# Optimization experiments

Hardware: AMD Instinct MI355X
Metric: run time of the kernel (lower is better)

The kernel has to match this reference:

```python
import jax, jax.numpy as jnp
import numpy as np

K = 10
NEG_SLOPE = 0.2


def _knn(x, k):
    # x: (B, C, N) -> idx (B, N, k) of k nearest neighbors (smallest sq-dist)
    inner = -2.0 * jnp.einsum('bcn,bcm->bnm', x, x)
    xx = jnp.sum(x * x, axis=1)  # (B, N)
    pd = -xx[:, :, None] - inner - xx[:, None, :]  # negative squared distance
    return jax.lax.top_k(pd, k)[1]


def _gather(xt, idx):
    # xt: (B, N, C), idx: (B, N, k) -> (B, N, k, C)
    return jax.vmap(lambda f, i: f[i])(xt, idx)


def graph_feature(x, k):
    # x: (B, C, N) -> (B, 2C, N, k)
    idx = _knn(x, k)
    xt = jnp.transpose(x, (0, 2, 1))  # (B, N, C)
    feat = _gather(xt, idx)           # (B, N, k, C)
    xc = xt[:, :, None, :]
    out = jnp.concatenate([feat - xc, jnp.broadcast_to(xc, feat.shape)], axis=3)
    return jnp.transpose(out, (0, 3, 1, 2))


def graph_feature1(x, k):
    # knn on first 2 dims (2D coords); x: (B, C, N) -> (B, 2C, N, k)
    idx = _knn(x[:, 0:2, :], k)
    xt = jnp.transpose(x, (0, 2, 1))
    feat = _gather(xt, idx)
    xc = jnp.broadcast_to(xt[:, :, None, :], feat.shape)
    out = jnp.concatenate([feat[..., :2] - xc[..., :2], feat[..., 2:], xc], axis=3)
    return jnp.transpose(out, (0, 3, 1, 2))


def _lrelu(v):
    return jnp.where(v >= 0, v, NEG_SLOPE * v)


def _cbr2(f, W, s, t):
    # 1x1 conv2d + folded-BN + leaky relu; f: (B, C, N, k)
    y = jnp.einsum('oc,bcnk->bonk', W, f)
    return _lrelu(y * s[None, :, None, None] + t[None, :, None, None])


def _cbr1(f, W, s, t):
    # 1x1 conv1d + folded-BN + leaky relu; f: (B, C, N)
    y = jnp.einsum('oc,bcn->bon', W, f)
    return _lrelu(y * s[None, :, None] + t[None, :, None])


def setup_inputs() -> dict:
    key = jax.random.key(0)
    ks = jax.random.split(key, 32)
    B, C, N = 8, 7, 4096
    d = {'x': jax.random.normal(ks[0], (B, C, N), jnp.float32)}
    wshapes = [('W1', (64, 14)), ('W2', (64, 64)), ('W3', (64, 128)), ('W4', (64, 64)),
               ('W5', (64, 128)), ('W6', (256, 192)), ('W7', (512, 448)), ('W8', (128, 1024))]
    for i, (n, s) in enumerate(wshapes):
        d[n] = jax.random.normal(ks[1 + i], s, jnp.float32) * (1.0 / np.sqrt(s[1]))
    bdims = [64, 64, 64, 64, 64, 256, 512, 128]
    for i, c in enumerate(bdims):
        d[f's{i + 1}'] = jax.random.uniform(ks[9 + i], (c,), jnp.float32, 0.5, 1.5)
        d[f't{i + 1}'] = jax.random.normal(ks[17 + i], (c,), jnp.float32) * 0.1
    return d


def reference(x, W1, W2, W3, W4, W5, W6, W7, W8,
              s1, s2, s3, s4, s5, s6, s7, s8,
              t1, t2, t3, t4, t5, t6, t7, t8):
    B, _, N = x.shape
    h = graph_feature1(x, K)              # (B, 14, N, K)
    h = _cbr2(h, W1, s1, t1)
    h = _cbr2(h, W2, s2, t2)
    x1 = h.mean(axis=-1)                  # (B, 64, N)
    h = graph_feature(x1, K)              # (B, 128, N, K)
    h = _cbr2(h, W3, s3, t3)
    h = _cbr2(h, W4, s4, t4)
    x2 = h.mean(axis=-1)
    h = graph_feature(x2, K)
    h = _cbr2(h, W5, s5, t5)
    x3 = h.mean(axis=-1)
    h = jnp.concatenate([x1, x2, x3], axis=1)   # (B, 192, N)
    h = _cbr1(h, W6, s6, t6)                    # (B, 256, N)
    g = h.mean(axis=-1, keepdims=True)          # (B, 256, 1)
    g = jnp.broadcast_to(g, (B, 256, N))
    h = jnp.concatenate([g, x1, x2, x3], axis=1)  # (B, 448, N)
    h = _cbr1(h, W7, s7, t7)                      # (B, 512, N)
    x4 = h.max(axis=-1)
    x5 = h.mean(axis=-1)
    h = jnp.concatenate([x4, x5], axis=1)         # (B, 1024)
    h = h @ W8.T                                  # (B, 128)
    return _lrelu(h * s8[None, :] + t8[None, :])
```

## Files before the change

### kernel.cpp

```cpp
#include <hip/hip_runtime.h>

#define BB 8
#define NN 4096
#define KK 10
#define CAP 24
#define TT 6
typedef unsigned long long u64;
typedef __attribute__((ext_vector_type(8))) short bf16x8;
typedef __attribute__((ext_vector_type(4))) float f32x4;

__device__ __forceinline__ float lrelu(float v){ return v >= 0.f ? v : 0.2f*v; }
__device__ __forceinline__ float bc(float v, int l){
  return __int_as_float(__builtin_amdgcn_readlane(__float_as_int(v), l));
}
__device__ __forceinline__ unsigned fenc(float f){
  unsigned u = __float_as_uint(f);
  return u ^ (((unsigned)((int)u >> 31)) | 0x80000000u);
}
__device__ __forceinline__ float fdec(unsigned e){
  return (e & 0x80000000u) ? __uint_as_float(e & 0x7fffffffu) : __uint_as_float(~e);
}
__device__ __forceinline__ u64 shflx_u64(u64 x, int d){
  unsigned lo = __shfl_xor((unsigned)x, d, 64);
  unsigned hi = __shfl_xor((unsigned)(x >> 32), d, 64);
  return ((u64)hi << 32) | lo;
}

__global__ __launch_bounds__(256) void prep_k(
    const float* __restrict__ W1, const float* __restrict__ W2, const float* __restrict__ W3,
    const float* __restrict__ W4, const float* __restrict__ W5, const float* __restrict__ W8,
    float* __restrict__ W1T, float* __restrict__ W2T, float* __restrict__ W5T, float* __restrict__ W8T,
    unsigned short* __restrict__ W3dh, unsigned short* __restrict__ W3dl,
    unsigned short* __restrict__ W3qh, unsigned short* __restrict__ W3ql,
    unsigned short* __restrict__ W4h,  unsigned short* __restrict__ W4l)
{
  const int t = blockIdx.x*256 + threadIdx.x;
  const int stride = gridDim.x*256;
  for (int i=t; i<64*14; i+=stride){ int o=i/14, c=i%14; W1T[c*64+o]=W1[i]; }
  for (int i=t; i<64*64; i+=stride){ int o=i>>6, c=i&63; W2T[c*64+o]=W2[i]; }
  for (int i=t; i<64*128; i+=stride){ int o=i>>7, c=i&127; W5T[c*64+o]=W5[i]; }
  for (int i=t; i<128*1024; i+=stride){ int o=i>>10, c=i&1023; W8T[c*128+o]=W8[i]; }
  for (int i=t; i<64*64; i+=stride){
    int o=i>>6, c=i&63;
    float f = W3[o*128 + c];
    unsigned u = __float_as_uint(f);
    W3dh[i] = (unsigned short)(u >> 16);
    float lo = f - __uint_as_float(u & 0xffff0000u);
    W3dl[i] = (unsigned short)(__float_as_uint(lo) >> 16);
  }
  for (int i=t; i<64*64; i+=stride){
    int o=i>>6, c=i&63;
    float f = W3[o*128 + 64 + c];
    unsigned u = __float_as_uint(f);
    W3qh[i] = (unsigned short)(u >> 16);
    float lo = f - __uint_as_float(u & 0xffff0000u);
    W3ql[i] = (unsigned short)(__float_as_uint(lo) >> 16);
  }
  for (int i=t; i<64*64; i+=stride){
    float f = W4[i];
    unsigned u = __float_as_uint(f);
    W4h[i] = (unsigned short)(u >> 16);
    float lo = f - __uint_as_float(u & 0xffff0000u);
    W4l[i] = (unsigned short)(__float_as_uint(lo) >> 16);
  }
}

__global__ __launch_bounds__(256) void cvt_k(const float* __restrict__ xin,
    unsigned short* __restrict__ Xh, unsigned short* __restrict__ Xl, float* __restrict__ xx)
{
  const int gid = blockIdx.x*256 + threadIdx.x;
  const int p = gid >> 3, c8 = (gid & 7) << 3;
  const float* src = xin + (size_t)p*64 + c8;
  float fv[8];
  *(float4*)&fv[0] = *(const float4*)(src);
  *(float4*)&fv[4] = *(const float4*)(src + 4);
  unsigned hp[4], lp[4];
  float ssq = 0.f;
  #pragma unroll
  for (int e=0; e<4; e++){
    float f0 = fv[2*e], f1 = fv[2*e+1];
    ssq += f0*f0 + f1*f1;
    unsigned u0 = __float_as_uint(f0), u1 = __float_as_uint(f1);
    hp[e] = (u0 >> 16) | (u1 & 0xffff0000u);
    float l0 = f0 - __uint_as_float(u0 & 0xffff0000u);
    float l1 = f1 - __uint_as_float(u1 & 0xffff0000u);
    lp[e] = (__float_as_uint(l0) >> 16) | (__float_as_uint(l1) & 0xffff0000u);
  }
  *(uint4*)(Xh + (size_t)p*64 + c8) = uint4{hp[0],hp[1],hp[2],hp[3]};
  *(uint4*)(Xl + (size_t)p*64 + c8) = uint4{lp[0],lp[1],lp[2],lp[3]};
  ssq += __shfl_xor(ssq, 1, 64);
  ssq += __shfl_xor(ssq, 2, 64);
  ssq += __shfl_xor(ssq, 4, 64);
  if ((gid & 7) == 0) xx[p] = ssq;
}

__global__ __launch_bounds__(256) void knn2d_k(const float* __restrict__ x, u64* __restrict__ pk)
{
  __shared__ float px[1024], py[1024], pxx[1024];
  __shared__ unsigned cnt[64];
  __shared__ u64 lst[64][CAP];
  const int tid = threadIdx.x;
  const int b  = blockIdx.x >> 8;
  const int qt = (blockIdx.x >> 2) & 63;
  const int h  = blockIdx.x & 3;
  const int q0 = qt*64;
  const int m0g = h*1024;
  const float* xb = x + (size_t)b*7*NN;
  for (int m = tid; m < 1024; m += 256){
    float a = xb[m0g + m], c = xb[NN + m0g + m];
    px[m] = a; py[m] = c; pxx[m] = a*a + c*c;
  }
  if (tid < 64) cnt[tid] = 0;
  __syncthreads();

  const int ty = tid >> 4, tx = tid & 15;
  const int qr = ty*4;
  float qx4[4], qy4[4], q24[4];
  #pragma unroll
  for (int i=0;i<4;i++){
    float a = xb[q0+qr+i], c = xb[NN + q0+qr+i];
    qx4[i] = a; qy4[i] = c; q24[i] = a*a + c*c;
  }

  float bv[4][TT];
  #pragma unroll
  for (int i=0;i<4;i++){
    #pragma unroll
    for (int s=0;s<TT;s++) bv[i][s] = -__builtin_inff();
  }

  for (int ot=0; ot<8; ot++){
    #pragma unroll
    for (int j=0;j<8;j++){
      const int ml = ot*128 + j*16 + tx;
      const float cmx = px[ml], cmy = py[ml], cm2 = pxx[ml];
      #pragma unroll
      for (int i=0;i<4;i++){
        float dot = qx4[i]*cmx + qy4[i]*cmy;
        float v = (-q24[i]) - (-2.f*dot) - cm2;
        float c = v;
        #pragma unroll
        for (int s=0;s<TT;s++){
          float nb = fmaxf(bv[i][s], c);
          c = fminf(bv[i][s], c);
          bv[i][s] = nb;
        }
      }
    }
  }

  float thr[4];
  #pragma unroll
  for (int i=0;i<4;i++){
    float m = 0.f;
    #pragma unroll
    for (int k=0;k<10;k++){
      float hh = bv[i][0];
      m = hh;
      m = fmaxf(m, __shfl_xor(m, 1, 64));
      m = fmaxf(m, __shfl_xor(m, 2, 64));
      m = fmaxf(m, __shfl_xor(m, 4, 64));
      m = fmaxf(m, __shfl_xor(m, 8, 64));
      if (k < 9){
        if (hh == m){
          #pragma unroll
          for (int s=0;s<TT-1;s++) bv[i][s] = bv[i][s+1];
          bv[i][TT-1] = -__builtin_inff();
        }
      }
    }
    thr[i] = m;
  }

  for (int ot=0; ot<8; ot++){
    #pragma unroll
    for (int j=0;j<8;j++){
      const int ml = ot*128 + j*16 + tx;
      const float cmx = px[ml], cmy = py[ml], cm2 = pxx[ml];
      const unsigned mk = ~(unsigned)(m0g + ml);
      #pragma unroll
      for (int i=0;i<4;i++){
        float dot = qx4[i]*cmx + qy4[i]*cmy;
        float v = (-q24[i]) - (-2.f*dot) - cm2;
        if (v >= thr[i]){
          u64 key = ((u64)fenc(v) << 32) | mk;
          const int r = qr + i;
          unsigned slot = atomicAdd(&cnt[r], 1u);
          if (slot < CAP) lst[r][slot] = key;
        }
      }
    }
  }
  __syncthreads();

  if (tid < 64){
    int n = (int)cnt[tid]; if (n > CAP) n = CAP;
    u64* L = lst[tid];
    u64* op = pk + (((size_t)b*NN + q0 + tid)*4 + h)*KK;
    for (int k=0;k<KK;k++){
      u64 best = 0ull; int bi = 0;
      for (int s=0;s<n;s++){
        u64 v2 = L[s];
        if (v2 > best){ best = v2; bi = s; }
      }
      if (best) L[bi] = 0ull;
      op[k] = best;
    }
  }
}

__global__ __launch_bounds__(256) void knn64_k(const unsigned short* __restrict__ Xh,
    const unsigned short* __restrict__ Xl, const float* __restrict__ xx, u64* __restrict__ pk)
{
  __shared__ unsigned short Ch[64*72], Cl[64*72];
  __shared__ float cxx[64];
  __shared__ unsigned cnt[64];
  __shared__ u64 lst[64][CAP];
  const int tid = threadIdx.x;
  const int b  = blockIdx.x >> 8;
  const int qt = (blockIdx.x >> 2) & 63;
  const int h  = blockIdx.x & 3;
  const int q0 = qt*64;
  const int m0g = h*1024;
  const unsigned short* Xhb = Xh + (size_t)b*NN*64;
  const unsigned short* Xlb = Xl + (size_t)b*NN*64;
  const float* xxb = xx + (size_t)b*NN;

  const int sp = tid >> 2;
  const int sc = (tid & 3) << 4;

  const int lane = tid & 63;
  const int w    = tid >> 6;
  const int col  = lane & 15;
  const int quad = (tid >> 4) & 3;
  const int qr   = (tid >> 4)*4;

  const size_t abase = (size_t)(q0 + w*16 + col)*64 + quad*8;
  bf16x8 Ah0 = *(const bf16x8*)(Xhb + abase);
  bf16x8 Ah1 = *(const bf16x8*)(Xhb + abase + 32);
  bf16x8 Al0 = *(const bf16x8*)(Xlb + abase);
  bf16x8 Al1 = *(const bf16x8*)(Xlb + abase + 32);

  float qx4[4];
  #pragma unroll
  for (int i=0;i<4;i++) qx4[i] = xxb[q0 + qr + i];

  if (tid < 64) cnt[tid] = 0;

  float bv[4][TT];
  #pragma unroll
  for (int i=0;i<4;i++){
    #pragma unroll
    for (int s=0;s<TT;s++) bv[i][s] = -__builtin_inff();
  }

  for (int ct=0; ct<16; ct++){
    const int m0 = m0g + ct*64;
    __syncthreads();
    {
      const uint4* sh = (const uint4*)(Xhb + (size_t)(m0+sp)*64 + sc);
      const uint4* sl = (const uint4*)(Xlb + (size_t)(m0+sp)*64 + sc);
      uint4 h0 = sh[0], h1 = sh[1], l0 = sl[0], l1 = sl[1];
      *(uint4*)(&Ch[sp*72 + sc])     = h0;
      *(uint4*)(&Ch[sp*72 + sc + 8]) = h1;
      *(uint4*)(&Cl[sp*72 + sc])     = l0;
      *(uint4*)(&Cl[sp*72 + sc + 8]) = l1;
      if (tid < 64) cxx[tid] = xxb[m0 + tid];
    }
    __syncthreads();

    #pragma unroll
    for (int j=0;j<4;j++){
      const int boff = (j*16 + col)*72 + quad*8;
      bf16x8 Bh0 = *(const bf16x8*)(&Ch[boff]);
      bf16x8 Bh1 = *(const bf16x8*)(&Ch[boff+32]);
      bf16x8 Bl0 = *(const bf16x8*)(&Cl[boff]);
      bf16x8 Bl1 = *(const bf16x8*)(&Cl[boff+32]);
      f32x4 d = {0.f,0.f,0.f,0.f};
      d = __builtin_amdgcn_mfma_f32_16x16x32_bf16(Al0, Bh0, d, 0,0,0);
      d = __builtin_amdgcn_mfma_f32_16x16x32_bf16(Ah0, Bl0, d, 0,0,0);
      d = __builtin_amdgcn_mfma_f32_16x16x32_bf16(Ah0, Bh0, d, 0,0,0);
      d = __builtin_amdgcn_mfma_f32_16x16x32_bf16(Al1, Bh1, d, 0,0,0);
      d = __builtin_amdgcn_mfma_f32_16x16x32_bf16(Ah1, Bl1, d, 0,0,0);
      d = __builtin_amdgcn_mfma_f32_16x16x32_bf16(Ah1, Bh1, d, 0,0,0);

      const float cx = cxx[j*16 + col];
      #pragma unroll
      for (int i=0;i<4;i++){
        float v = (-qx4[i]) - (-2.f*d[i]) - cx;
        float c = v;
        #pragma unroll
        for (int s=0;s<TT;s++){
          float nb = fmaxf(bv[i][s], c);
          c = fminf(bv[i][s], c);
          bv[i][s] = nb;
        }
      }
    }
  }

  float thr[4];
  #pragma unroll
  for (int i=0;i<4;i++){
    float m = 0.f;
    #pragma unroll
    for (int k=0;k<10;k++){
      float hh = bv[i][0];
      m = hh;
      m = fmaxf(m, __shfl_xor(m, 1, 64));
      m = fmaxf(m, __shfl_xor(m, 2, 64));
      m = fmaxf(m, __shfl_xor(m, 4, 64));
      m = fmaxf(m, __shfl_xor(m, 8, 64));
      if (k < 9){
        if (hh == m){
          #pragma unroll
          for (int s=0;s<TT-1;s++) bv[i][s] = bv[i][s+1];
          bv[i][TT-1] = -__builtin_inff();
        }
      }
    }
    thr[i] = m;
  }

  for (int ct=0; ct<16; ct++){
    const int m0 = m0g + ct*64;
    __syncthreads();
    {
      const uint4* sh = (const uint4*)(Xhb + (size_t)(m0+sp)*64 + sc);
      const uint4* sl = (const uint4*)(Xlb + (size_t)(m0+sp)*64 + sc);
      uint4 h0 = sh[0], h1 = sh[1], l0 = sl[0], l1 = sl[1];
      *(uint4*)(&Ch[sp*72 + sc])     = h0;
      *(uint4*)(&Ch[sp*72 + sc + 8]) = h1;
      *(uint4*)(&Cl[sp*72 + sc])     = l0;
      *(uint4*)(&Cl[sp*72 + sc + 8]) = l1;
      if (tid < 64) cxx[tid] = xxb[m0 + tid];
    }
    __syncthreads();

    #pragma unroll
    for (int j=0;j<4;j++){
      const int boff = (j*16 + col)*72 + quad*8;
      bf16x8 Bh0 = *(const bf16x8*)(&Ch[boff]);
      bf16x8 Bh1 = *(const bf16x8*)(&Ch[boff+32]);
      bf16x8 Bl0 = *(const bf16x8*)(&Cl[boff]);
      bf16x8 Bl1 = *(const bf16x8*)(&Cl[boff+32]);
      f32x4 d = {0.f,0.f,0.f,0.f};
      d = __builtin_amdgcn_mfma_f32_16x16x32_bf16(Al0, Bh0, d, 0,0,0);
      d = __builtin_amdgcn_mfma_f32_16x16x32_bf16(Ah0, Bl0, d, 0,0,0);
      d = __builtin_amdgcn_mfma_f32_16x16x32_bf16(Ah0, Bh0, d, 0,0,0);
      d = __builtin_amdgcn_mfma_f32_16x16x32_bf16(Al1, Bh1, d, 0,0,0);
      d = __builtin_amdgcn_mfma_f32_16x16x32_bf16(Ah1, Bl1, d, 0,0,0);
      d = __builtin_amdgcn_mfma_f32_16x16x32_bf16(Ah1, Bh1, d, 0,0,0);

      const int m = m0 + j*16 + col;
      const float cx = cxx[j*16 + col];
      const unsigned mk = ~(unsigned)m;
      #pragma unroll
      for (int i=0;i<4;i++){
        float v = (-qx4[i]) - (-2.f*d[i]) - cx;
        if (v >= thr[i]){
          u64 key = ((u64)fenc(v) << 32) | mk;
          const int r = qr + i;
          unsigned slot = atomicAdd(&cnt[r], 1u);
          if (slot < CAP) lst[r][slot] = key;
        }
      }
    }
  }
  __syncthreads();

  if (tid < 64){
    int n = (int)cnt[tid]; if (n > CAP) n = CAP;
    u64* L = lst[tid];
    u64* op = pk + (((size_t)b*NN + q0 + tid)*4 + h)*KK;
    for (int k=0;k<KK;k++){
      u64 best = 0ull; int bi = 0;
      for (int s=0;s<n;s++){
        u64 v2 = L[s];
        if (v2 > best){ best = v2; bi = s; }
      }
      if (best) L[bi] = 0ull;
      op[k] = best;
    }
  }
}

__global__ __launch_bounds__(256) void kmerge_k(const u64* __restrict__ pk, int* __restrict__ idxo)
{
  const int q = blockIdx.x*256 + threadIdx.x;
  const u64* A = pk + (size_t)q*(4*KK);
  int* op = idxo + (size_t)q*KK;
  int ia = 0, ib = 0, ic = 0, id = 0;
  #pragma unroll
  for (int k=0;k<KK;k++){
    u64 a  = (ia < KK) ? A[ia]        : 0ull;
    u64 b2 = (ib < KK) ? A[KK + ib]   : 0ull;
    u64 c2 = (ic < KK) ? A[2*KK + ic] : 0ull;
    u64 d2 = (id < KK) ? A[3*KK + id] : 0ull;
    u64 m1 = a >= b2 ? a : b2;  int s1 = a >= b2 ? 0 : 1;
    u64 m2 = c2 >= d2 ? c2 : d2; int s2 = c2 >= d2 ? 2 : 3;
    u64 mm = m1 >= m2 ? m1 : m2; int ss = m1 >= m2 ? s1 : s2;
    op[k] = (int)(~(unsigned)mm);
    if (ss == 0) ia++; else if (ss == 1) ib++; else if (ss == 2) ic++; else id++;
  }
}

__global__ __launch_bounds__(256) void edge1_k(const float* __restrict__ x, const int* __restrict__ idx,
    const float* __restrict__ W1T, const float* __restrict__ W2T,
    const float* __restrict__ s1, const float* __restrict__ t1,
    const float* __restrict__ s2, const float* __restrict__ t2,
    float* __restrict__ x1t)
{
  const int lane = threadIdx.x & 63;
  const int pt = (blockIdx.x << 2) + (threadIdx.x >> 6);
  const int b = pt >> 12, n = pt & 4095;
  const float* xb = x + (size_t)b*7*NN;
  float w1r[14], w2r[64];
  #pragma unroll
  for (int c=0;c<14;c++) w1r[c] = W1T[c*64 + lane];
  #pragma unroll
  for (int c=0;c<64;c++) w2r[c] = W2T[c*64 + lane];
  const float s1o=s1[lane], t1o=t1[lane], s2o=s2[lane], t2o=t2[lane];
  const float xq = (lane < 7) ? xb[lane*NN + n] : 0.f;
  const float xq0 = bc(xq,0), xq1 = bc(xq,1);
  float qy1 = 0.f;
  #pragma unroll
  for (int c=0;c<7;c++) qy1 += w1r[7+c]*bc(xq,c);
  const int* ip = idx + (size_t)pt*KK;
  float acc = 0.f;
  for (int j=0;j<KK;j++){
    const int ij = ip[j];
    const float xg = (lane < 7) ? xb[lane*NN + ij] : 0.f;
    float y1 = qy1;
    y1 += w1r[0]*(bc(xg,0) - xq0);
    y1 += w1r[1]*(bc(xg,1) - xq1);
    #pragma unroll
    for (int c=2;c<7;c++) y1 += w1r[c]*bc(xg,c);
    const float z1 = lrelu(y1*s1o + t1o);
    float p0=0.f,p1=0.f,p2=0.f,p3=0.f;
    #pragma unroll
    for (int c=0;c<64;c+=4){
      p0 += w2r[c+0]*bc(z1,c+0);
      p1 += w2r[c+1]*bc(z1,c+1);
      p2 += w2r[c+2]*bc(z1,c+2);
      p3 += w2r[c+3]*bc(z1,c+3);
    }
    acc += lrelu(((p0+p1)+(p2+p3))*s2o + t2o);
  }
  x1t[(size_t)pt*64 + lane] = acc / 10.f;
}

__global__ __launch_bounds__(256) void edge2_k(const float* __restrict__ x1t, const int* __restrict__ idx,
    const unsigned short* __restrict__ W3dh, const unsigned short* __restrict__ W3dl,
    const unsigned short* __restrict__ W3qh, const unsigned short* __restrict__ W3ql,
    const unsigned short* __restrict__ W4h,  const unsigned short* __restrict__ W4l,
    const float* __restrict__ s3, const float* __restrict__ t3,
    const float* __restrict__ s4, const float* __restrict__ t4,
    float* __restrict__ xout)
{
  __shared__ unsigned short Zh[80*72], Zl[80*72];
  __shared__ unsigned short Qh[16*72], Ql[16*72];
  __shared__ float accf[64*8];
  const int tid = threadIdx.x;
  const size_t p0 = (size_t)blockIdx.x * 8;

  ((float2*)accf)[tid] = float2{0.f, 0.f};

  #pragma unroll
  for (int pass=0; pass<2; ++pass){
    const int col = pass*64 + (tid>>2);
    const int sc16 = (tid&3)*16;
    if (col < 88){
      float dv[16];
      if (col < 80){
        const int p = col/10, j = col - p*10;
        const size_t pt = p0 + p;
        const int bb = (int)(pt >> 12);
        const int ij = idx[pt*KK + j];
        const float* gs = x1t + ((size_t)bb*NN + ij)*64 + sc16;
        const float* qs = x1t + pt*64 + sc16;
        #pragma unroll
        for (int e=0;e<4;e++){
          float4 g4 = *(const float4*)(gs + e*4);
          float4 q4 = *(const float4*)(qs + e*4);
          dv[e*4+0]=g4.x-q4.x; dv[e*4+1]=g4.y-q4.y; dv[e*4+2]=g4.z-q4.z; dv[e*4+3]=g4.w-q4.w;
        }
      } else {
        const int cl = col - 80;
        const float* qs = x1t + (size_t)(p0+cl)*64 + sc16;
        #pragma unroll
        for (int e=0;e<4;e++){
          float4 q4 = *(const float4*)(qs + e*4);
          dv[e*4+0]=q4.x; dv[e*4+1]=q4.y; dv[e*4+2]=q4.z; dv[e*4+3]=q4.w;
        }
      }
      unsigned hp[8], lp[8];
      #pragma unroll
      for (int e=0;e<8;e++){
        float f0 = dv[2*e], f1 = dv[2*e+1];
        unsigned u0 = __float_as_uint(f0), u1 = __float_as_uint(f1);
        hp[e] = (u0 >> 16) | (u1 & 0xffff0000u);
        float l0 = f0 - __uint_as_float(u0 & 0xffff0000u);
        float l1 = f1 - __uint_as_float(u1 & 0xffff0000u);
        lp[e] = (__float_as_uint(l0) >> 16) | (__float_as_uint(l1) & 0xffff0000u);
      }
      if (col < 80){
        *(uint4*)(&Zh[col*72 + sc16])     = uint4{hp[0],hp[1],hp[2],hp[3]};
        *(uint4*)(&Zh[col*72 + sc16 + 8]) = uint4{hp[4],hp[5],hp[6],hp[7]};
        *(uint4*)(&Zl[col*72 + sc16])     = uint4{lp[0],lp[1],lp[2],lp[3]};
        *(uint4*)(&Zl[col*72 + sc16 + 8]) = uint4{lp[4],lp[5],lp[6],lp[7]};
      } else {
        const int cl = col - 80;
        *(uint4*)(&Qh[cl*72 + sc16])     = uint4{hp[0],hp[1],hp[2],hp[3]};
        *(uint4*)(&Qh[cl*72 + sc16 + 8]) = uint4{hp[4],hp[5],hp[6],hp[7]};
        *(uint4*)(&Ql[cl*72 + sc16])     = uint4{lp[0],lp[1],lp[2],lp[3]};
        *(uint4*)(&Ql[cl*72 + sc16 + 8]) = uint4{lp[4],lp[5],lp[6],lp[7]};
      }
    } else if (col < 96){
      const int cl = col - 80;
      const uint4 z{0u,0u,0u,0u};
      *(uint4*)(&Qh[cl*72 + sc16])     = z;
      *(uint4*)(&Qh[cl*72 + sc16 + 8]) = z;
      *(uint4*)(&Ql[cl*72 + sc16])     = z;
      *(uint4*)(&Ql[cl*72 + sc16 + 8]) = z;
    }
  }
  __syncthreads();

  const int lane = tid & 63;
  const int w    = tid >> 6;
  const int colL = lane & 15;
  const int quad = lane >> 4;
  const int arow = (w*16 + colL)*64 + quad*8;

  bf16x8 Adh0 = *(const bf16x8*)(W3dh + arow);
  bf16x8 Adh1 = *(const bf16x8*)(W3dh + arow + 32);
  bf16x8 Adl0 = *(const bf16x8*)(W3dl + arow);
  bf16x8 Adl1 = *(const bf16x8*)(W3dl + arow + 32);

  f32x4 C1[5];
  #pragma unroll
  for (int t=0;t<5;t++){
    const int boff = (t*16 + colL)*72 + quad*8;
    bf16x8 Bh0 = *(const bf16x8*)(&Zh[boff]);
    bf16x8 Bh1 = *(const bf16x8*)(&Zh[boff+32]);
    bf16x8 Bl0 = *(const bf16x8*)(&Zl[boff]);
    bf16x8 Bl1 = *(const bf16x8*)(&Zl[boff+32]);
    f32x4 d = {0.f,0.f,0.f,0.f};
    d = __builtin_amdgcn_mfma_f32_16x16x32_bf16(Adl0, Bh0, d, 0,0,0);
    d = __builtin_amdgcn_mfma_f32_16x16x32_bf16(Adh0, Bl0, d, 0,0,0);
    d = __builtin_amdgcn_mfma_f32_16x16x32_bf16(Adh0, Bh0, d, 0,0,0);
    d = __builtin_amdgcn_mfma_f32_16x16x32_bf16(Adl1, Bh1, d, 0,0,0);
    d = __builtin_amdgcn_mfma_f32_16x16x32_bf16(Adh1, Bl1, d, 0,0,0);
    d = __builtin_amdgcn_mfma_f32_16x16x32_bf16(Adh1, Bh1, d, 0,0,0);
    C1[t] = d;
  }
  f32x4 Cu;
  {
    bf16x8 Aqh0 = *(const bf16x8*)(W3qh + arow);
    bf16x8 Aqh1 = *(const bf16x8*)(W3qh + arow + 32);
    bf16x8 Aql0 = *(const bf16x8*)(W3ql + arow);
    bf16x8 Aql1 = *(const bf16x8*)(W3ql + arow + 32);
    const int boff = colL*72 + quad*8;
    bf16x8 Bh0 = *(const bf16x8*)(&Qh[boff]);
    bf16x8 Bh1 = *(const bf16x8*)(&Qh[boff+32]);
    bf16x8 Bl0 = *(const bf16x8*)(&Ql[boff]);
    bf16x8 Bl1 = *(const bf16x8*)(&Ql[boff+32]);
    f32x4 d = {0.f,0.f,0.f,0.f};
    d = __builtin_amdgcn_mfma_f32_16x16x32_bf16(Aql0, Bh0, d, 0,0,0);
    d = __builtin_amdgcn_mfma_f32_16x16x32_bf16(Aqh0, Bl0, d, 0,0,0);
    d = __builtin_amdgcn_mfma_f32_16x16x32_bf16(Aqh0, Bh0, d, 0,0,0);
    d = __builtin_amdgcn_mfma_f32_16x16x32_bf16(Aql1, Bh1, d, 0,0,0);
    d = __builtin_amdgcn_mfma_f32_16x16x32_bf16(Aqh1, Bl1, d, 0,0,0);
    d = __builtin_amdgcn_mfma_f32_16x16x32_bf16(Aqh1, Bh1, d, 0,0,0);
    Cu = d;
  }

  float s3v[4], t3v[4], s4v[4], t4v[4];
  #pragma unroll
  for (int i=0;i<4;i++){
    const int o = w*16 + quad*4 + i;
    s3v[i]=s3[o]; t3v[i]=t3[o]; s4v[i]=s4[o]; t4v[i]=t4[o];
  }

  __syncthreads();

  #pragma unroll
  for (int t=0;t<5;t++){
    const int gc = t*16 + colL;
    const int p  = gc/10;
    const int srcb = (((lane & 48) | p) << 2);
    float z[4];
    #pragma unroll
    for (int i=0;i<4;i++){
      float ui = __int_as_float(__builtin_amdgcn_ds_bpermute(srcb, __float_as_int(Cu[i])));
      float zp = (C1[t][i] + ui)*s3v[i] + t3v[i];
      z[i] = zp >= 0.f ? zp : 0.2f*zp;
    }
    unsigned u0=__float_as_uint(z[0]), u1=__float_as_uint(z[1]);
    unsigned u2=__float_as_uint(z[2]), u3=__float_as_uint(z[3]);
    unsigned h01 = (u0>>16) | (u1 & 0xffff0000u);
    unsigned h23 = (u2>>16) | (u3 & 0xffff0000u);
    float l0 = z[0]-__uint_as_float(u0&0xffff0000u);
    float l1 = z[1]-__uint_as_float(u1&0xffff0000u);
    float l2 = z[2]-__uint_as_float(u2&0xffff0000u);
    float l3 = z[3]-__uint_as_float(u3&0xffff0000u);
    unsigned l01 = (__float_as_uint(l0)>>16) | (__float_as_uint(l1)&0xffff0000u);
    unsigned l23 = (__float_as_uint(l2)>>16) | (__float_as_uint(l3)&0xffff0000u);
    const int rb = w*16 + quad*4;
    *(uint2*)(&Zh[gc*72 + rb]) = uint2{h01,h23};
    *(uint2*)(&Zl[gc*72 + rb]) = uint2{l01,l23};
  }
  __syncthreads();

  bf16x8 A4h0 = *(const bf16x8*)(W4h + arow);
  bf16x8 A4h1 = *(const bf16x8*)(W4h + arow + 32);
  bf16x8 A4l0 = *(const bf16x8*)(W4l + arow);
  bf16x8 A4l1 = *(const bf16x8*)(W4l + arow + 32);
  #pragma unroll
  for (int t=0;t<5;t++){
    const int boff = (t*16 + colL)*72 + quad*8;
    bf16x8 Bh0 = *(const bf16x8*)(&Zh[boff]);
    bf16x8 Bh1 = *(const bf16x8*)(&Zh[boff+32]);
    bf16x8 Bl0 = *(const bf16x8*)(&Zl[boff]);
    bf16x8 Bl1 = *(const bf16x8*)(&Zl[boff+32]);
    f32x4 d = {0.f,0.f,0.f,0.f};
    d = __builtin_amdgcn_mfma_f32_16x16x32_bf16(A4l0, Bh0, d, 0,0,0);
    d = __builtin_amdgcn_mfma_f32_16x16x32_bf16(A4h0, Bl0, d, 0,0,0);
    d = __builtin_amdgcn_mfma_f32_16x16x32_bf16(A4h0, Bh0, d, 0,0,0);
    d = __builtin_amdgcn_mfma_f32_16x16x32_bf16(A4l1, Bh1, d, 0,0,0);
    d = __builtin_amdgcn_mfma_f32_16x16x32_bf16(A4h1, Bl1, d, 0,0,0);
    d = __builtin_amdgcn_mfma_f32_16x16x32_bf16(A4h1, Bh1, d, 0,0,0);
    const int gc = t*16 + colL;
    const int p  = gc/10;
    #pragma unroll
    for (int i=0;i<4;i++){
      float v = d[i]*s4v[i] + t4v[i];
      v = v >= 0.f ? v : 0.2f*v;
      atomicAdd(&accf[(w*16 + quad*4 + i)*8 + p], v);
    }
  }
  __syncthreads();

  {
    const int o = tid & 63;
    #pragma unroll
    for (int g=0; g<2; ++g){
      const int p = (tid>>6) + g*4;
      xout[(p0+p)*64 + o] = accf[o*8+p] / 10.f;
    }
  }
}

__global__ __launch_bounds__(256) void edge3_k(const float* __restrict__ xin, const int* __restrict__ idx,
    const float* __restrict__ W5T,
    const float* __restrict__ s5, const float* __restrict__ t5,
    float* __restrict__ xout)
{
  const int lane = threadIdx.x & 63;
  const int pt = (blockIdx.x << 2) + (threadIdx.x >> 6);
  const int b = pt >> 12;
  float wd[64], wq[64];
  #pragma unroll
  for (int c=0;c<64;c++) wd[c] = W5T[c*64 + lane];
  #pragma unroll
  for (int c=0;c<64;c++) wq[c] = W5T[(64+c)*64 + lane];
  const float s5o=s5[lane], t5o=t5[lane];
  const float xq = xin[(size_t)pt*64 + lane];
  float a0=0.f,a1=0.f,a2=0.f,a3=0.f;
  #pragma unroll
  for (int c=0;c<64;c+=4){
    a0 += wq[c+0]*bc(xq,c+0);
    a1 += wq[c+1]*bc(xq,c+1);
    a2 += wq[c+2]*bc(xq,c+2);
    a3 += wq[c+3]*bc(xq,c+3);
  }
  const float yq = (a0+a1)+(a2+a3);
  const int* ip = idx + (size_t)pt*KK;
  float acc = 0.f;
  for (int j=0;j<KK;j++){
    const int ij = ip[j];
    const float xg = xin[((size_t)(b*NN + ij))*64 + lane];
    const float d = xg - xq;
    float p0=0.f,p1=0.f,p2=0.f,p3=0.f;
    #pragma unroll
    for (int c=0;c<64;c+=4){
      p0 += wd[c+0]*bc(d,c+0);
      p1 += wd[c+1]*bc(d,c+1);
      p2 += wd[c+2]*bc(d,c+2);
      p3 += wd[c+3]*bc(d,c+3);
    }
    acc += lrelu((yq + ((p0+p1)+(p2+p3)))*s5o + t5o);
  }
  xout[(size_t)pt*64 + lane] = acc / 10.f;
}

__global__ __launch_bounds__(256) void g1_k(const float* __restrict__ W6,
   const float* __restrict__ x1t, const float* __restrict__ x2t, const float* __restrict__ x3t,
   const float* __restrict__ s6, const float* __restrict__ t6, float* __restrict__ gsum)
{
  __shared__ float Wl[16*132];
  __shared__ float Zl[16*260];
  const int tid = threadIdx.x;
  const int rb = blockIdx.x & 1;
  const int nt = (blockIdx.x >> 1) & 15;
  const int b  = blockIdx.x >> 5;
  const int r0 = rb*128;
  const int n0 = nt*256;
  const int ty = tid >> 4, tx = tid & 15;
  float acc[8][16];
  #pragma unroll
  for (int i=0;i<8;i++){
    #pragma unroll
    for (int j=0;j<16;j++) acc[i][j] = 0.f;
  }
  for (int kc=0; kc<12; kc++){
    __syncthreads();
    {
      const int r = tid >> 1, h = tid & 1;
      const float4* wp = (const float4*)(W6 + (size_t)(r0 + r)*192 + kc*16 + h*8);
      float tmp[8];
      *(float4*)&tmp[0] = wp[0];
      *(float4*)&tmp[4] = wp[1];
      #pragma unroll
      for (int u=0;u<8;u++) Wl[(h*8+u)*132 + r] = tmp[u];
    }
    {
      const float* arr = (kc < 4) ? x1t : (kc < 8) ? x2t : x3t;
      const int chofs = (kc & 3)*16;
      const float4* zp = (const float4*)(arr + ((size_t)(b*NN) + n0 + tid)*64 + chofs);
      float tmp[16];
      *(float4*)&tmp[0]  = zp[0];
      *(float4*)&tmp[4]  = zp[1];
      *(float4*)&tmp[8]  = zp[2];
      *(float4*)&tmp[12] = zp[3];
      #pragma unroll
      for (int u=0;u<16;u++) Zl[u*260 + tid] = tmp[u];
    }
    __syncthreads();
    #pragma unroll 4
    for (int k=0;k<16;k++){
      float wv[8], zv[16];
      *(float4*)&wv[0] = *(const float4*)(&Wl[k*132 + ty*8]);
      *(float4*)&wv[4] = *(const float4*)(&Wl[k*132 + ty*8 + 4]);
      #pragma unroll
      for (int jg=0;jg<4;jg++)
        *(float4*)&zv[jg*4] = *(const float4*)(&Zl[k*260 + jg*64 + tx*4]);
      #pragma unroll
      for (int i=0;i<8;i++){
        #pragma unroll
        for (int j=0;j<16;j++) acc[i][j] += wv[i]*zv[j];
      }
    }
  }
  #pragma unroll
  for (int i=0;i<8;i++){
    const int row = r0 + ty*8 + i;
    const float sv = s6[row], tv = t6[row];
    float sum = 0.f;
    #pragma unroll
    for (int j=0;j<16;j++) sum += lrelu(acc[i][j]*sv + tv);
    #pragma unroll
    for (int d=1; d<16; d<<=1) sum += __shfl_xor(sum, d, 64);
    if ((tid & 15) == 0) atomicAdd(&gsum[b*256 + row], sum);
  }
}

__global__ __launch_bounds__(256) void g2_k(const float* __restrict__ W7,
   const float* __restrict__ gsum, float* __restrict__ c7)
{
  const int b = blockIdx.x >> 1;
  const int o = (blockIdx.x & 1)*256 + threadIdx.x;
  const float* wr = W7 + (size_t)o*448;
  const float* gb = gsum + b*256;
  float a0=0.f,a1=0.f,a2=0.f,a3=0.f;
  #pragma unroll 4
  for (int c=0;c<256;c+=4){
    a0 += wr[c+0]*gb[c+0]; a1 += wr[c+1]*gb[c+1];
    a2 += wr[c+2]*gb[c+2]; a3 += wr[c+3]*gb[c+3];
  }
  c7[b*512+o] = ((a0+a1)+(a2+a3)) * (1.f/4096.f);
}

__global__ __launch_bounds__(256) void g3_k(const float* __restrict__ W7,
   const float* __restrict__ x1t, const float* __restrict__ x2t, const float* __restrict__ x3t,
   const float* __restrict__ c7, const float* __restrict__ s7, const float* __restrict__ t7,
   unsigned* __restrict__ x4e, float* __restrict__ x5s)
{
  __shared__ float Wl[16*132];
  __shared__ float Zl[16*260];
  const int tid = threadIdx.x;
  const int rb = blockIdx.x & 3;
  const int nt = (blockIdx.x >> 2) & 15;
  const int b  = blockIdx.x >> 6;
  const int r0 = rb*128;
  const int n0 = nt*256;
  const int ty = tid >> 4, tx = tid & 15;
  float acc[8][16];
  #pragma unroll
  for (int i=0;i<8;i++){
    #pragma unroll
    for (int j=0;j<16;j++) acc[i][j] = 0.f;
  }
  for (int kc=0; kc<12; kc++){
    __syncthreads();
    {
      const int r = tid >> 1, h = tid & 1;
      const float4* wp = (const float4*)(W7 + (size_t)(r0 + r)*448 + 256 + kc*16 + h*8);
      float tmp[8];
      *(float4*)&tmp[0] = wp[0];
      *(float4*)&tmp[4] = wp[1];
      #pragma unroll
      for (int u=0;u<8;u++) Wl[(h*8+u)*132 + r] = tmp[u];
    }
    {
      const float* arr = (kc < 4) ? x1t : (kc < 8) ? x2t : x3t;
      const int chofs = (kc & 3)*16;
      const float4* zp = (const float4*)(arr + ((size_t)(b*NN) + n0 + tid)*64 + chofs);
      float tmp[16];
      *(float4*)&tmp[0]  = zp[0];
      *(float4*)&tmp[4]  = zp[1];
      *(float4*)&tmp[8]  = zp[2];
      *(float4*)&tmp[12] = zp[3];
      #pragma unroll
      for (int u=0;u<16;u++) Zl[u*260 + tid] = tmp[u];
    }
    __syncthreads();
    #pragma unroll 4
    for (int k=0;k<16;k++){
      float wv[8], zv[16];
      *(float4*)&wv[0] = *(const float4*)(&Wl[k*132 + ty*8]);
      *(float4*)&wv[4] = *(const float4*)(&Wl[k*132 + ty*8 + 4]);
      #pragma unroll
      for (int jg=0;jg<4;jg++)
        *(float4*)&zv[jg*4] = *(const float4*)(&Zl[k*260 + jg*64 + tx*4]);
      #pragma unroll
      for (int i=0;i<8;i++){
        #pragma unroll
        for (int j=0;j<16;j++) acc[i][j] += wv[i]*zv[j];
      }
    }
  }
  #pragma unroll
  for (int i=0;i<8;i++){
    const int row = r0 + ty*8 + i;
    const float c7v = c7[b*512 + row];
    const float sv = s7[row], tv = t7[row];
    float mx = -__builtin_inff(), sum = 0.f;
    #pragma unroll
    for (int j=0;j<16;j++){
      float h = lrelu((acc[i][j] + c7v)*sv + tv);
      mx = fmaxf(mx, h); sum += h;
    }
    #pragma unroll
    for (int d=1; d<16; d<<=1){
      sum += __shfl_xor(sum, d, 64);
      mx = fmaxf(mx, __shfl_xor(mx, d, 64));
    }
    if ((tid & 15) == 0){
      atomicAdd(&x5s[b*512 + row], sum);
      atomicMax(&x4e[b*512 + row], fenc(mx));
    }
  }
}

__global__ __launch_bounds__(128) void g4_k(const float* __restrict__ W8T,
  const unsigned* __restrict__ x4e, const float* __restrict__ x5s,
  const float* __restrict__ s8, const float* __restrict__ t8, float* __restrict__ out)
{
  const int b = blockIdx.x, j = threadIdx.x;
  float a0 = 0.f, a1 = 0.f;
  for (int o=0;o<512;o++){
    a0 += W8T[o*128 + j] * fdec(x4e[b*512 + o]);
    a1 += W8T[(512+o)*128 + j] * (x5s[b*512 + o] * (1.f/4096.f));
  }
  const float y = a0 + a1;
  out[b*128 + j] = lrelu(y*s8[j] + t8[j]);
}

extern "C" void kernel_launch(void* const* d_in, const int* in_sizes, int n_in,
                              void* d_out, int out_size, void* d_ws, size_t ws_size,
                              hipStream_t stream) {
  (void)in_sizes; (void)n_in; (void)out_size; (void)ws_size;
  const float* x  = (const float*)d_in[0];
  const float* W1 = (const float*)d_in[1];
  const float* W2 = (const float*)d_in[2];
  const float* W3 = (const float*)d_in[3];
  const float* W4 = (const float*)d_in[4];
  const float* W5 = (const float*)d_in[5];
  const float* W6 = (const float*)d_in[6];
  const float* W7 = (const float*)d_in[7];
  const float* W8 = (const float*)d_in[8];
  const float* s1 = (const float*)d_in[9];   const float* t1 = (const float*)d_in[10];
  const float* s2 = (const float*)d_in[11];  const float* t2 = (const float*)d_in[12];
  const float* s3 = (const float*)d_in[13];  const float* t3 = (const float*)d_in[14];
  const float* s4 = (const float*)d_in[15];  const float* t4 = (const float*)d_in[16];
  const float* s5 = (const float*)d_in[17];  const float* t5 = (const float*)d_in[18];
  const float* s6 = (const float*)d_in[19];  const float* t6 = (const float*)d_in[20];
  const float* s7 = (const float*)d_in[21];  const float* t7 = (const float*)d_in[22];
  const float* s8 = (const float*)d_in[23];  const float* t8 = (const float*)d_in[24];

  char* wsb = (char*)d_ws;
  size_t off = 0;
  auto alloc = [&](size_t bytes)->char* {
    char* p = wsb + off;
    off += (bytes + 255) & ~(size_t)255;
    return p;
  };
  int*      idx1 = (int*)alloc((size_t)BB*NN*KK*4);
  int*      idx2 = (int*)alloc((size_t)BB*NN*KK*4);
  int*      idx3 = (int*)alloc((size_t)BB*NN*KK*4);
  u64*      pkeys= (u64*)alloc((size_t)BB*NN*4*KK*8);
  float*    x1t  = (float*)alloc((size_t)BB*NN*64*4);
  float*    x2t  = (float*)alloc((size_t)BB*NN*64*4);
  float*    x3t  = (float*)alloc((size_t)BB*NN*64*4);
  unsigned short* Xh = (unsigned short*)alloc((size_t)BB*NN*64*2);
  unsigned short* Xl = (unsigned short*)alloc((size_t)BB*NN*64*2);
  float*    xxb  = (float*)alloc((size_t)BB*NN*4);
  float*    gsum = (float*)alloc((size_t)BB*256*4);
  unsigned* x4e  = (unsigned*)alloc((size_t)BB*512*4);
  float*    x5s  = (float*)alloc((size_t)BB*512*4);
  float*    c7   = (float*)alloc((size_t)BB*512*4);
  float*    W1T  = (float*)alloc(14*64*4);
  float*    W2T  = (float*)alloc(64*64*4);
  float*    W5T  = (float*)alloc(128*64*4);
  float*    W8T  = (float*)alloc(1024*128*4);
  unsigned short* W3dh = (unsigned short*)alloc(64*64*2);
  unsigned short* W3dl = (unsigned short*)alloc(64*64*2);
  unsigned short* W3qh = (unsigned short*)alloc(64*64*2);
  unsigned short* W3ql = (unsigned short*)alloc(64*64*2);
  unsigned short* W4h  = (unsigned short*)alloc(64*64*2);
  unsigned short* W4l  = (unsigned short*)alloc(64*64*2);

  prep_k<<<64,256,0,stream>>>(W1,W2,W3,W4,W5,W8, W1T,W2T,W5T,W8T, W3dh,W3dl,W3qh,W3ql,W4h,W4l);
  knn2d_k<<<BB*64*4,256,0,stream>>>(x, pkeys);
  kmerge_k<<<BB*NN/256,256,0,stream>>>(pkeys, idx1);
  edge1_k<<<BB*NN/4,256,0,stream>>>(x, idx1, W1T, W2T, s1,t1,s2,t2, x1t);
  cvt_k<<<BB*NN*8/256,256,0,stream>>>(x1t, Xh, Xl, xxb);
  knn64_k<<<BB*64*4,256,0,stream>>>(Xh, Xl, xxb, pkeys);
  kmerge_k<<<BB*NN/256,256,0,stream>>>(pkeys, idx2);
  edge2_k<<<BB*NN/8,256,0,stream>>>(x1t, idx2, W3dh,W3dl,W3qh,W3ql,W4h,W4l, s3,t3,s4,t4, x2t);
  cvt_k<<<BB*NN*8/256,256,0,stream>>>(x2t, Xh, Xl, xxb);
  knn64_k<<<BB*64*4,256,0,stream>>>(Xh, Xl, xxb, pkeys);
  kmerge_k<<<BB*NN/256,256,0,stream>>>(pkeys, idx3);
  edge3_k<<<BB*NN/4,256,0,stream>>>(x2t, idx3, W5T, s5,t5, x3t);
  hipMemsetAsync(gsum, 0, (size_t)BB*256*4 + (size_t)BB*512*4*2, stream);
  g1_k<<<256,256,0,stream>>>(W6, x1t,x2t,x3t, s6,t6, gsum);
  g2_k<<<16,256,0,stream>>>(W7, gsum, c7);
  g3_k<<<512,256,0,stream>>>(W7, x1t,x2t,x3t, c7, s7,t7, x4e, x5s);
  g4_k<<<BB,128,0,stream>>>(W8T, x4e, x5s, s8,t8, (float*)d_out);
}
```

Baseline: 1.106 ms.

## Rewrite edge3 with split-bf16 MFMA and transpose kNN candidate lists

The edge3 conv stage moves from per-lane scalar FMAs with readlane broadcasts to MFMA matrix instructions. It splits W5 and the gathered edge differences into high and low bf16 halves (three-product emulation) and processes 8 points (80 edges) per block. The kNN candidate lists in shared memory are transposed to [slot][row], so that the serial top-k scan by 64 threads avoids bank conflicts. TT changes from 6 to 4. Accuracy depends on the bf16x3 split, and results are accumulated with shared-memory float atomics.

```diff
diff --git a/kernel.cpp b/kernel.cpp
--- a/kernel.cpp
+++ b/kernel.cpp
@@ -4,7 +4,7 @@
 #define NN 4096
 #define KK 10
 #define CAP 24
-#define TT 6
+#define TT 4
 typedef unsigned long long u64;
 typedef __attribute__((ext_vector_type(8))) short bf16x8;
 typedef __attribute__((ext_vector_type(4))) float f32x4;
@@ -20,25 +20,21 @@
 __device__ __forceinline__ float fdec(unsigned e){
   return (e & 0x80000000u) ? __uint_as_float(e & 0x7fffffffu) : __uint_as_float(~e);
 }
-__device__ __forceinline__ u64 shflx_u64(u64 x, int d){
-  unsigned lo = __shfl_xor((unsigned)x, d, 64);
-  unsigned hi = __shfl_xor((unsigned)(x >> 32), d, 64);
-  return ((u64)hi << 32) | lo;
-}
 
 __global__ __launch_bounds__(256) void prep_k(
     const float* __restrict__ W1, const float* __restrict__ W2, const float* __restrict__ W3,
     const float* __restrict__ W4, const float* __restrict__ W5, const float* __restrict__ W8,
-    float* __restrict__ W1T, float* __restrict__ W2T, float* __restrict__ W5T, float* __restrict__ W8T,
+    float* __restrict__ W1T, float* __restrict__ W2T, float* __restrict__ W8T,
     unsigned short* __restrict__ W3dh, unsigned short* __restrict__ W3dl,
     unsigned short* __restrict__ W3qh, unsigned short* __restrict__ W3ql,
-    unsigned short* __restrict__ W4h,  unsigned short* __restrict__ W4l)
+    unsigned short* __restrict__ W4h,  unsigned short* __restrict__ W4l,
+    unsigned short* __restrict__ W5dh, unsigned short* __restrict__ W5dl,
+    unsigned short* __restrict__ W5qh, unsigned short* __restrict__ W5ql)
 {
   const int t = blockIdx.x*256 + threadIdx.x;
   const int stride = gridDim.x*256;
   for (int i=t; i<64*14; i+=stride){ int o=i/14, c=i%14; W1T[c*64+o]=W1[i]; }
   for (int i=t; i<64*64; i+=stride){ int o=i>>6, c=i&63; W2T[c*64+o]=W2[i]; }
-  for (int i=t; i<64*128; i+=stride){ int o=i>>7, c=i&127; W5T[c*64+o]=W5[i]; }
   for (int i=t; i<128*1024; i+=stride){ int o=i>>10, c=i&1023; W8T[c*128+o]=W8[i]; }
   for (int i=t; i<64*64; i+=stride){
     int o=i>>6, c=i&63;
@@ -63,6 +59,22 @@
     float lo = f - __uint_as_float(u & 0xffff0000u);
     W4l[i] = (unsigned short)(__float_as_uint(lo) >> 16);
   }
+  for (int i=t; i<64*64; i+=stride){
+    int o=i>>6, c=i&63;
+    float f = W5[o*128 + c];
+    unsigned u = __float_as_uint(f);
+    W5dh[i] = (unsigned short)(u >> 16);
+    float lo = f - __uint_as_float(u & 0xffff0000u);
+    W5dl[i] = (unsigned short)(__float_as_uint(lo) >> 16);
+  }
+  for (int i=t; i<64*64; i+=stride){
+    int o=i>>6, c=i&63;
+    float f = W5[o*128 + 64 + c];
+    unsigned u = __float_as_uint(f);
+    W5qh[i] = (unsigned short)(u >> 16);
+    float lo = f - __uint_as_float(u & 0xffff0000u);
+    W5ql[i] = (unsigned short)(__float_as_uint(lo) >> 16);
+  }
 }
 
 __global__ __launch_bounds__(256) void cvt_k(const float* __restrict__ xin,
@@ -98,7 +110,7 @@
 {
   __shared__ float px[1024], py[1024], pxx[1024];
   __shared__ unsigned cnt[64];
-  __shared__ u64 lst[64][CAP];
+  __shared__ u64 lst[CAP][64];
   const int tid = threadIdx.x;
   const int b  = blockIdx.x >> 8;
   const int qt = (blockIdx.x >> 2) & 63;
@@ -186,7 +198,7 @@
           u64 key = ((u64)fenc(v) << 32) | mk;
           const int r = qr + i;
           unsigned slot = atomicAdd(&cnt[r], 1u);
-          if (slot < CAP) lst[r][slot] = key;
+          if (slot < CAP) lst[slot][r] = key;
         }
       }
     }
@@ -195,15 +207,14 @@
 
   if (tid < 64){
     int n = (int)cnt[tid]; if (n > CAP) n = CAP;
-    u64* L = lst[tid];
     u64* op = pk + (((size_t)b*NN + q0 + tid)*4 + h)*KK;
     for (int k=0;k<KK;k++){
       u64 best = 0ull; int bi = 0;
       for (int s=0;s<n;s++){
-        u64 v2 = L[s];
+        u64 v2 = lst[s][tid];
         if (v2 > best){ best = v2; bi = s; }
       }
-      if (best) L[bi] = 0ull;
+      if (best) lst[bi][tid] = 0ull;
       op[k] = best;
     }
   }
@@ -215,7 +226,7 @@
   __shared__ unsigned short Ch[64*72], Cl[64*72];
   __shared__ float cxx[64];
   __shared__ unsigned cnt[64];
-  __shared__ u64 lst[64][CAP];
+  __shared__ u64 lst[CAP][64];
   const int tid = threadIdx.x;
   const int b  = blockIdx.x >> 8;
   const int qt = (blockIdx.x >> 2) & 63;
@@ -362,7 +373,7 @@
           u64 key = ((u64)fenc(v) << 32) | mk;
           const int r = qr + i;
           unsigned slot = atomicAdd(&cnt[r], 1u);
-          if (slot < CAP) lst[r][slot] = key;
+          if (slot < CAP) lst[slot][r] = key;
         }
       }
     }
@@ -371,15 +382,14 @@
 
   if (tid < 64){
     int n = (int)cnt[tid]; if (n > CAP) n = CAP;
-    u64* L = lst[tid];
     u64* op = pk + (((size_t)b*NN + q0 + tid)*4 + h)*KK;
     for (int k=0;k<KK;k++){
       u64 best = 0ull; int bi = 0;
       for (int s=0;s<n;s++){
-        u64 v2 = L[s];
+        u64 v2 = lst[s][tid];
         if (v2 > best){ best = v2; bi = s; }
       }
-      if (best) L[bi] = 0ull;
+      if (best) lst[bi][tid] = 0ull;
       op[k] = best;
     }
   }
@@ -653,46 +663,159 @@
 }
 
 __global__ __launch_bounds__(256) void edge3_k(const float* __restrict__ xin, const int* __restrict__ idx,
-    const float* __restrict__ W5T,
+    const unsigned short* __restrict__ W5dh, const unsigned short* __restrict__ W5dl,
+    const unsigned short* __restrict__ W5qh, const unsigned short* __restrict__ W5ql,
     const float* __restrict__ s5, const float* __restrict__ t5,
     float* __restrict__ xout)
 {
-  const int lane = threadIdx.x & 63;
-  const int pt = (blockIdx.x << 2) + (threadIdx.x >> 6);
-  const int b = pt >> 12;
-  float wd[64], wq[64];
-  #pragma unroll
-  for (int c=0;c<64;c++) wd[c] = W5T[c*64 + lane];
-  #pragma unroll
-  for (int c=0;c<64;c++) wq[c] = W5T[(64+c)*64 + lane];
-  const float s5o=s5[lane], t5o=t5[lane];
-  const float xq = xin[(size_t)pt*64 + lane];
-  float a0=0.f,a1=0.f,a2=0.f,a3=0.f;
-  #pragma unroll
-  for (int c=0;c<64;c+=4){
-    a0 += wq[c+0]*bc(xq,c+0);
-    a1 += wq[c+1]*bc(xq,c+1);
-    a2 += wq[c+2]*bc(xq,c+2);
-    a3 += wq[c+3]*bc(xq,c+3);
-  }
-  const float yq = (a0+a1)+(a2+a3);
-  const int* ip = idx + (size_t)pt*KK;
-  float acc = 0.f;
-  for (int j=0;j<KK;j++){
-    const int ij = ip[j];
-    const float xg = xin[((size_t)(b*NN + ij))*64 + lane];
-    const float d = xg - xq;
-    float p0=0.f,p1=0.f,p2=0.f,p3=0.f;
-    #pragma unroll
-    for (int c=0;c<64;c+=4){
-      p0 += wd[c+0]*bc(d,c+0);
-      p1 += wd[c+1]*bc(d,c+1);
-      p2 += wd[c+2]*bc(d,c+2);
-      p3 += wd[c+3]*bc(d,c+3);
-    }
-    acc += lrelu((yq + ((p0+p1)+(p2+p3)))*s5o + t5o);
-  }
-  xout[(size_t)pt*64 + lane] = acc / 10.f;
+  __shared__ unsigned short Zh[80*72], Zl[80*72];
+  __shared__ unsigned short Qh[16*72], Ql[16*72];
+  __shared__ float accf[64*8];
+  const int tid = threadIdx.x;
+  const size_t p0 = (size_t)blockIdx.x * 8;
+
+  ((float2*)accf)[tid] = float2{0.f, 0.f};
+
+  #pragma unroll
+  for (int pass=0; pass<2; ++pass){
+    const int col = pass*64 + (tid>>2);
+    const int sc16 = (tid&3)*16;
+    if (col < 88){
+      float dv[16];
+      if (col < 80){
+        const int p = col/10, j = col - p*10;
+        const size_t pt = p0 + p;
+        const int bb = (int)(pt >> 12);
+        const int ij = idx[pt*KK + j];
+        const float* gs = xin + ((size_t)bb*NN + ij)*64 + sc16;
+        const float* qs = xin + pt*64 + sc16;
+        #pragma unroll
+        for (int e=0;e<4;e++){
+          float4 g4 = *(const float4*)(gs + e*4);
+          float4 q4 = *(const float4*)(qs + e*4);
+          dv[e*4+0]=g4.x-q4.x; dv[e*4+1]=g4.y-q4.y; dv[e*4+2]=g4.z-q4.z; dv[e*4+3]=g4.w-q4.w;
+        }
+      } else {
+        const int cl = col - 80;
+        const float* qs = xin + (size_t)(p0+cl)*64 + sc16;
+        #pragma unroll
+        for (int e=0;e<4;e++){
+          float4 q4 = *(const float4*)(qs + e*4);
+          dv[e*4+0]=q4.x; dv[e*4+1]=q4.y; dv[e*4+2]=q4.z; dv[e*4+3]=q4.w;
+        }
+      }
+      unsigned hp[8], lp[8];
+      #pragma unroll
+      for (int e=0;e<8;e++){
+        float f0 = dv[2*e], f1 = dv[2*e+1];
+        unsigned u0 = __float_as_uint(f0), u1 = __float_as_uint(f1);
+        hp[e] = (u0 >> 16) | (u1 & 0xffff0000u);
+        float l0 = f0 - __uint_as_float(u0 & 0xffff0000u);
+        float l1 = f1 - __uint_as_float(u1 & 0xffff0000u);
+        lp[e] = (__float_as_uint(l0) >> 16) | (__float_as_uint(l1) & 0xffff0000u);
+      }
+      if (col < 80){
+        *(uint4*)(&Zh[col*72 + sc16])     = uint4{hp[0],hp[1],hp[2],hp[3]};
+        *(uint4*)(&Zh[col*72 + sc16 + 8]) = uint4{hp[4],hp[5],hp[6],hp[7]};
+        *(uint4*)(&Zl[col*72 + sc16])     = uint4{lp[0],lp[1],lp[2],lp[3]};
+        *(uint4*)(&Zl[col*72 + sc16 + 8]) = uint4{lp[4],lp[5],lp[6],lp[7]};
+      } else {
+        const int cl = col - 80;
+        *(uint4*)(&Qh[cl*72 + sc16])     = uint4{hp[0],hp[1],hp[2],hp[3]};
+        *(uint4*)(&Qh[cl*72 + sc16 + 8]) = uint4{hp[4],hp[5],hp[6],hp[7]};
+        *(uint4*)(&Ql[cl*72 + sc16])     = uint4{lp[0],lp[1],lp[2],lp[3]};
+        *(uint4*)(&Ql[cl*72 + sc16 + 8]) = uint4{lp[4],lp[5],lp[6],lp[7]};
+      }
+    } else if (col < 96){
+      const int cl = col - 80;
+      const uint4 z{0u,0u,0u,0u};
+      *(uint4*)(&Qh[cl*72 + sc16])     = z;
+      *(uint4*)(&Qh[cl*72 + sc16 + 8]) = z;
+      *(uint4*)(&Ql[cl*72 + sc16])     = z;
+      *(uint4*)(&Ql[cl*72 + sc16 + 8]) = z;
+    }
+  }
+  __syncthreads();
+
+  const int lane = tid & 63;
+  const int w    = tid >> 6;
+  const int colL = lane & 15;
+  const int quad = lane >> 4;
+  const int arow = (w*16 + colL)*64 + quad*8;
+
+  bf16x8 Adh0 = *(const bf16x8*)(W5dh + arow);
+  bf16x8 Adh1 = *(const bf16x8*)(W5dh + arow + 32);
+  bf16x8 Adl0 = *(const bf16x8*)(W5dl + arow);
+  bf16x8 Adl1 = *(const bf16x8*)(W5dl + arow + 32);
+
+  f32x4 C1[5];
+  #pragma unroll
+  for (int t=0;t<5;t++){
+    const int boff = (t*16 + colL)*72 + quad*8;
+    bf16x8 Bh0 = *(const bf16x8*)(&Zh[boff]);
+    bf16x8 Bh1 = *(const bf16x8*)(&Zh[boff+32]);
+    bf16x8 Bl0 = *(const bf16x8*)(&Zl[boff]);
+    bf16x8 Bl1 = *(const bf16x8*)(&Zl[boff+32]);
+    f32x4 d = {0.f,0.f,0.f,0.f};
+    d = __builtin_amdgcn_mfma_f32_16x16x32_bf16(Adl0, Bh0, d, 0,0,0);
+    d = __builtin_amdgcn_mfma_f32_16x16x32_bf16(Adh0, Bl0, d, 0,0,0);
+    d = __builtin_amdgcn_mfma_f32_16x16x32_bf16(Adh0, Bh0, d, 0,0,0);
+    d = __builtin_amdgcn_mfma_f32_16x16x32_bf16(Adl1, Bh1, d, 0,0,0);
+    d = __builtin_amdgcn_mfma_f32_16x16x32_bf16(Adh1, Bl1, d, 0,0,0);
+    d = __builtin_amdgcn_mfma_f32_16x16x32_bf16(Adh1, Bh1, d, 0,0,0);
+    C1[t] = d;
+  }
+  f32x4 Cu;
+  {
+    bf16x8 Aqh0 = *(const bf16x8*)(W5qh + arow);
+    bf16x8 Aqh1 = *(const bf16x8*)(W5qh + arow + 32);
+    bf16x8 Aql0 = *(const bf16x8*)(W5ql + arow);
+    bf16x8 Aql1 = *(const bf16x8*)(W5ql + arow + 32);
+    const int boff = colL*72 + quad*8;
+    bf16x8 Bh0 = *(const bf16x8*)(&Qh[boff]);
+    bf16x8 Bh1 = *(const bf16x8*)(&Qh[boff+32]);
+    bf16x8 Bl0 = *(const bf16x8*)(&Ql[boff]);
+    bf16x8 Bl1 = *(const bf16x8*)(&Ql[boff+32]);
+    f32x4 d = {0.f,0.f,0.f,0.f};
+    d = __builtin_amdgcn_mfma_f32_16x16x32_bf16(Aql0, Bh0, d, 0,0,0);
+    d = __builtin_amdgcn_mfma_f32_16x16x32_bf16(Aqh0, Bl0, d, 0,0,0);
+    d = __builtin_amdgcn_mfma_f32_16x16x32_bf16(Aqh0, Bh0, d, 0,0,0);
+    d = __builtin_amdgcn_mfma_f32_16x16x32_bf16(Aql1, Bh1, d, 0,0,0);
+    d = __builtin_amdgcn_mfma_f32_16x16x32_bf16(Aqh1, Bl1, d, 0,0,0);
+    d = __builtin_amdgcn_mfma_f32_16x16x32_bf16(Aqh1, Bh1, d, 0,0,0);
+    Cu = d;
+  }
+
+  float s5v[4], t5v[4];
+  #pragma unroll
+  for (int i=0;i<4;i++){
+    const int o = w*16 + quad*4 + i;
+    s5v[i]=s5[o]; t5v[i]=t5[o];
+  }
+
+  #pragma unroll
+  for (int t=0;t<5;t++){
+    const int gc = t*16 + colL;
+    const int p  = gc/10;
+    const int srcb = (((lane & 48) | p) << 2);
+    #pragma unroll
+    for (int i=0;i<4;i++){
+      float ui = __int_as_float(__builtin_amdgcn_ds_bpermute(srcb, __float_as_int(Cu[i])));
+      float zp = (C1[t][i] + ui)*s5v[i] + t5v[i];
+      zp = zp >= 0.f ? zp : 0.2f*zp;
+      atomicAdd(&accf[(w*16 + quad*4 + i)*8 + p], zp);
+    }
+  }
+  __syncthreads();
+
+  {
+    const int o = tid & 63;
+    #pragma unroll
+    for (int g=0; g<2; ++g){
+      const int p = (tid>>6) + g*4;
+      xout[(p0+p)*64 + o] = accf[o*8+p] / 10.f;
+    }
+  }
 }
 
 __global__ __launch_bounds__(256) void g1_k(const float* __restrict__ W6,
@@ -923,7 +1046,6 @@
   float*    c7   = (float*)alloc((size_t)BB*512*4);
   float*    W1T  = (float*)alloc(14*64*4);
   float*    W2T  = (float*)alloc(64*64*4);
-  float*    W5T  = (float*)alloc(128*64*4);
   float*    W8T  = (float*)alloc(1024*128*4);
   unsigned short* W3dh = (unsigned short*)alloc(64*64*2);
   unsigned short* W3dl = (unsigned short*)alloc(64*64*2);
@@ -931,8 +1053,13 @@
   unsigned short* W3ql = (unsigned short*)alloc(64*64*2);
   unsigned short* W4h  = (unsigned short*)alloc(64*64*2);
   unsigned short* W4l  = (unsigned short*)alloc(64*64*2);
-
-  prep_k<<<64,256,0,stream>>>(W1,W2,W3,W4,W5,W8, W1T,W2T,W5T,W8T, W3dh,W3dl,W3qh,W3ql,W4h,W4l);
+  unsigned short* W5dh = (unsigned short*)alloc(64*64*2);
+  unsigned short* W5dl = (unsigned short*)alloc(64*64*2);
+  unsigned short* W5qh = (unsigned short*)alloc(64*64*2);
+  unsigned short* W5ql = (unsigned short*)alloc(64*64*2);
+
+  prep_k<<<64,256,0,stream>>>(W1,W2,W3,W4,W5,W8, W1T,W2T,W8T,
+                              W3dh,W3dl,W3qh,W3ql,W4h,W4l, W5dh,W5dl,W5qh,W5ql);
   knn2d_k<<<BB*64*4,256,0,stream>>>(x, pkeys);
   kmerge_k<<<BB*NN/256,256,0,stream>>>(pkeys, idx1);
   edge1_k<<<BB*NN/4,256,0,stream>>>(x, idx1, W1T, W2T, s1,t1,s2,t2, x1t);
@@ -943,7 +1070,7 @@
   cvt_k<<<BB*NN*8/256,256,0,stream>>>(x2t, Xh, Xl, xxb);
   knn64_k<<<BB*64*4,256,0,stream>>>(Xh, Xl, xxb, pkeys);
   kmerge_k<<<BB*NN/256,256,0,stream>>>(pkeys, idx3);
-  edge3_k<<<BB*NN/4,256,0,stream>>>(x2t, idx3, W5T, s5,t5, x3t);
+  edge3_k<<<BB*NN/8,256,0,stream>>>(x2t, idx3, W5dh,W5dl,W5qh,W5ql, s5,t5, x3t);
   hipMemsetAsync(gsum, 0, (size_t)BB*256*4 + (size_t)BB*512*4*2, stream);
   g1_k<<<256,256,0,stream>>>(W6, x1t,x2t,x3t, s6,t6, gsum);
   g2_k<<<16,256,0,stream>>>(W7, gsum, c7);
```

After: 1.129 ms. +2.0%, slower.
